# Kernel tuning notes

Measured on AMD Instinct MI355X. Metric: run time of the kernel, lower is better.

## Reference

```python
import jax, jax.numpy as jnp
import numpy as np
from jax import lax

CENTER_NUM = 2048


def setup_inputs() -> dict:
    key = jax.random.key(0)
    xyz = jax.random.normal(key, (32, 65536, 3), dtype=jnp.float32)
    return {"xyz": xyz}


def furthest_point_sample(xyz, m):
    """Iterative FPS. xyz: [B, N, 3] -> indices [B, m] (int32).

    Matches pointnet2_utils.furthest_point_sample: start at index 0,
    maintain running min squared distance to the selected set, pick argmax.
    """
    B, N, _ = xyz.shape
    init_idx = jnp.zeros((B,), dtype=jnp.int32)
    init_dists = jnp.full((B, N), 1e10, dtype=xyz.dtype)

    def step(carry, _):
        dists, last_idx = carry
        last = jnp.take_along_axis(xyz, last_idx[:, None, None], axis=1)  # [B,1,3]
        d = jnp.sum((xyz - last) ** 2, axis=-1)  # [B,N] squared dist to last center
        dists = jnp.minimum(dists, d)
        nxt = jnp.argmax(dists, axis=-1).astype(jnp.int32)  # [B]
        return (dists, nxt), nxt

    (_, _), rest = lax.scan(step, (init_dists, init_idx), None, length=m - 1)
    # rest: [m-1, B] -> prepend initial index, transpose to [B, m]
    idx = jnp.concatenate([init_idx[None, :], rest], axis=0).T
    return idx


def index_points(points, idx):
    """points: [B, N, C], idx: [B, m] -> [B, m, C]."""
    return jnp.take_along_axis(points, idx[..., None], axis=1)


def reference(xyz):
    fps_idx = furthest_point_sample(xyz, CENTER_NUM)  # [B, m]
    center_xyz = index_points(xyz, fps_idx)           # [B, m, 3]
    return center_xyz
```

## Files before the change

### kernel.cpp

```cpp
#include <hip/hip_runtime.h>
#include <stdint.h>

#define NBATCH 32
#define NPTS   65536
#define MCENT  2048
#define BPB    8
#define THREADS 1024
#define CHUNK  (NPTS / BPB)
#define WPT    (CHUNK / THREADS)
#define NWAVE  (THREADS / 64)
#define TMAX   64

typedef unsigned long long u64;
typedef uint32_t u32;

static __device__ __forceinline__ u32 fbits(float f) { union { float f; u32 u; } c; c.f = f; return c.u; }
static __device__ __forceinline__ float bitsf(u32 u) { union { u32 u; float f; } c; c.u = u; return c.f; }

static __device__ __forceinline__ u32 wave_max_u32(u32 v) {
#define STEP(CTRL) { const u32 o = (u32)__builtin_amdgcn_update_dpp(0, (int)v, CTRL, 0xF, 0xF, true); v = o > v ? o : v; }
    STEP(0x111)
    STEP(0x112)
    STEP(0x114)
    STEP(0x118)
    STEP(0x142)
    STEP(0x143)
#undef STEP
    return (u32)__builtin_amdgcn_readlane((int)v, 63);
}


template<int GPW>
__global__ __launch_bounds__(THREADS, 1) void fps_kernel(
    const float* __restrict__ xyz,
    float* __restrict__ out,
    u64* __restrict__ slots)
{
    constexpr int GROUPL = 64 / GPW;
    constexpr int POOLW  = BPB * NWAVE * GPW * 2;
    constexpr int WPL    = POOLW / 64;

    const int t = threadIdx.x;
    const int b = blockIdx.x >> 3;
    const int j = blockIdx.x & 7;
    const float* base = xyz + (size_t)b * NPTS * 3;
    const int p0 = j * CHUNK;
    const int wave = t >> 6;
    const int lane = t & 63;

    float px[WPT], py[WPT], pz[WPT], pd[WPT];
#pragma unroll
    for (int q = 0; q < WPT; ++q) {
        const int p = p0 + q * THREADS + t;
        px[q] = base[(size_t)p * 3 + 0];
        py[q] = base[(size_t)p * 3 + 1];
        pz[q] = base[(size_t)p * 3 + 2];
        pd[q] = 1e10f;
    }

    __shared__ float wcx[TMAX], wcy[TMAX], wcz[TMAX];
    __shared__ int   wcnt;

    if (t == 0) {
        const float cx = base[0], cy = base[1], cz = base[2];
        wcx[0] = cx; wcy[0] = cy; wcz[0] = cz; wcnt = 1;
        if (j == 0) {
            float* o = out + (size_t)b * MCENT * 3;
            o[0] = cx; o[1] = cy; o[2] = cz;
        }
    }

    int C = 0;
    for (int s = 1; ; ++s) {
        __syncthreads();
        const int tn = wcnt;
        C += tn;
        if (C >= MCENT) break;

        for (int tt = 0; tt < tn; ++tt) {
            const float cx = wcx[tt], cy = wcy[tt], cz = wcz[tt];
#pragma unroll
            for (int q = 0; q < WPT; ++q) {
                const float dx = __fsub_rn(px[q], cx);
                const float dy = __fsub_rn(py[q], cy);
                const float dz = __fsub_rn(pz[q], cz);
                const float s2 = __fmaf_rn(dz, dz,
                                 __fmaf_rn(dx, dx,
                                 __fmul_rn(dy, dy)));
                pd[q] = fminf(pd[q], s2);
            }
        }

        u64 k1 = 0, k2 = 0;
#pragma unroll
        for (int q = 0; q < WPT; ++q) {
            const u64 kk = ((u64)fbits(pd[q]) << 16)
                         | (u64)(0xFFFFu ^ (u32)(p0 + q * THREADS + t));
            if (kk > k1) { k2 = k1; k1 = kk; } else if (kk > k2) { k2 = kk; }
        }
#pragma unroll
        for (int m = 1; m <= GROUPL / 2; m <<= 1) {
            const u64 o1 = __shfl_xor(k1, m);
            const u64 o2 = __shfl_xor(k2, m);
            if (o1 > k1) { k2 = (k1 > o2) ? k1 : o2; k1 = o1; }
            else         { k2 = (k2 > o1) ? k2 : o1; }
        }

        u64* const bb = slots + ((size_t)(s & 1) * NBATCH + b) * POOLW;
        const u32 tag = (u32)s & 0xFFFFu;

        if ((lane & (GROUPL - 1)) == 0) {
            const int g = wave * GPW + lane / GROUPL;
            __hip_atomic_store(&bb[j * (NWAVE * GPW * 2) + g * 2 + 0],
                               (k1 << 16) | tag,
                               __ATOMIC_RELAXED, __HIP_MEMORY_SCOPE_AGENT);
            __hip_atomic_store(&bb[j * (NWAVE * GPW * 2) + g * 2 + 1],
                               (k2 << 16) | tag,
                               __ATOMIC_RELAXED, __HIP_MEMORY_SCOPE_AGENT);
        }

        if (wave == 0) {
            u64 w[WPL]; int ok;
            do {
#pragma unroll
                for (int r = 0; r < WPL; ++r)
                    w[r] = __hip_atomic_load(&bb[lane + 64 * r],
                                             __ATOMIC_RELAXED, __HIP_MEMORY_SCOPE_AGENT);
                ok = 1;
#pragma unroll
                for (int r = 0; r < WPL; ++r)
                    ok &= ((u32)(w[r] & 0xFFFFull) == tag);
            } while (!__all(ok));

            u32 pv[WPL], pi[WPL];
            float ex[WPL], ey[WPL], ez[WPL];
#pragma unroll
            for (int r = 0; r < WPL; ++r) {
                pv[r] = (u32)(w[r] >> 32);
                pi[r] = ((u32)w[r] >> 16) & 0xFFFFu;
                const int gi = (int)(0xFFFFu ^ pi[r]);
                ex[r] = base[(size_t)gi * 3 + 0];
                ey[r] = base[(size_t)gi * 3 + 1];
                ez[r] = base[(size_t)gi * 3 + 2];
            }

            u32 tl = 0;
#pragma unroll
            for (int r = 0; r < WPL; ++r) tl = pv[r] > tl ? pv[r] : tl;
            tl = (lane & 1) ? tl : 0u;
            const u32 tauv = wave_max_u32(tl);

            int tc = 0;
            while (1) {
                u32 lv = 0;
#pragma unroll
                for (int r = 0; r < WPL; ++r) lv = pv[r] > lv ? pv[r] : lv;
                const u32 vmax = wave_max_u32(lv);
                if (tc > 0 && vmax <= tauv) break;

                u32 ic = 0;
#pragma unroll
                for (int r = 0; r < WPL; ++r)
                    ic = (pv[r] == vmax && pi[r] + 1u > ic) ? pi[r] + 1u : ic;
                const u32 winv = wave_max_u32(ic) - 1u;

                float sx = 0.f, sy = 0.f, sz = 0.f; int mm = 0;
#pragma unroll
                for (int r = 0; r < WPL; ++r) {
                    const int m = (pv[r] == vmax) & (pi[r] == winv);
                    mm |= m;
                    sx = m ? ex[r] : sx;
                    sy = m ? ey[r] : sy;
                    sz = m ? ez[r] : sz;
                }
                const u64 bal = __ballot(mm);
                const int ol = (int)__ffsll((long long)bal) - 1;
                const float wx = __shfl(sx, ol);
                const float wy = __shfl(sy, ol);
                const float wz = __shfl(sz, ol);

                if (lane == 0) {
                    wcx[tc] = wx; wcy[tc] = wy; wcz[tc] = wz;
                    if (j == 0) {
                        float* o = out + ((size_t)b * MCENT + (C + tc)) * 3;
                        o[0] = wx; o[1] = wy; o[2] = wz;
                    }
                }
                ++tc;
                if (C + tc >= MCENT || tc >= TMAX) break;

#pragma unroll
                for (int r = 0; r < WPL; ++r) {
                    const float dx = __fsub_rn(ex[r], wx);
                    const float dy = __fsub_rn(ey[r], wy);
                    const float dz = __fsub_rn(ez[r], wz);
                    const float s2 = __fmaf_rn(dz, dz,
                                     __fmaf_rn(dx, dx,
                                     __fmul_rn(dy, dy)));
                    pv[r] = fbits(fminf(bitsf(pv[r]), s2));
                }
            }
            if (lane == 0) wcnt = tc;
        }
    }
}

extern "C" void kernel_launch(void* const* d_in, const int* in_sizes, int n_in,
                              void* d_out, int out_size, void* d_ws, size_t ws_size,
                              hipStream_t stream) {
    const float* xyz = (const float*)d_in[0];
    float* out = (float*)d_out;
    u64* slots = (u64*)d_ws;

    const size_t need_deep = 2ull * NBATCH * (BPB * NWAVE * 2 * 2) * sizeof(u64);
    if (ws_size >= need_deep) {
        fps_kernel<2><<<dim3(NBATCH * BPB), dim3(THREADS), 0, stream>>>(xyz, out, slots);
    } else {
        fps_kernel<1><<<dim3(NBATCH * BPB), dim3(THREADS), 0, stream>>>(xyz, out, slots);
    }
}
```

Before: 2.090 ms.

## Publish top-3 candidates per group to extract more centers per sync round

Each 32-lane group now keeps and merges a top-3 (instead of top-2) of its running-min distances and writes all three to the cross-block candidate pool. The pooled threshold is the max of the third-ranked entries, which should let more centers be selected per global synchronization round and so cut the number of inter-block barriers. It also adds a fast path for the winner lookup when only one lane holds the maximum, skipping a wave reduction. The cost is a heavier per-thread and per-shuffle merge, a larger pool for wave 0 to load and scan, and more stores per round.

```diff
diff --git a/kernel.cpp b/kernel.cpp
--- a/kernel.cpp
+++ b/kernel.cpp
@@ -9,6 +9,8 @@
 #define CHUNK  (NPTS / BPB)
 #define WPT    (CHUNK / THREADS)
 #define NWAVE  (THREADS / 64)
+#define GPW    2
+#define NGRP   (NWAVE * GPW)
 #define TMAX   64
 
 typedef unsigned long long u64;
@@ -30,15 +32,14 @@
 }
 
 
-template<int GPW>
+template<int TOPK>
 __global__ __launch_bounds__(THREADS, 1) void fps_kernel(
     const float* __restrict__ xyz,
     float* __restrict__ out,
     u64* __restrict__ slots)
 {
-    constexpr int GROUPL = 64 / GPW;
-    constexpr int POOLW  = BPB * NWAVE * GPW * 2;
-    constexpr int WPL    = POOLW / 64;
+    constexpr int POOLW = BPB * NGRP * TOPK;
+    constexpr int WPL   = POOLW / 64;
 
     const int t = threadIdx.x;
     const int b = blockIdx.x >> 3;
@@ -91,32 +92,51 @@
             }
         }
 
-        u64 k1 = 0, k2 = 0;
+        u64 k1 = 0, k2 = 0, k3 = 0;
 #pragma unroll
         for (int q = 0; q < WPT; ++q) {
             const u64 kk = ((u64)fbits(pd[q]) << 16)
                          | (u64)(0xFFFFu ^ (u32)(p0 + q * THREADS + t));
-            if (kk > k1) { k2 = k1; k1 = kk; } else if (kk > k2) { k2 = kk; }
-        }
-#pragma unroll
-        for (int m = 1; m <= GROUPL / 2; m <<= 1) {
+            if (kk > k1)      { k3 = k2; k2 = k1; k1 = kk; }
+            else if (kk > k2) { k3 = k2; k2 = kk; }
+            else if (kk > k3) { k3 = kk; }
+        }
+#pragma unroll
+        for (int m = 1; m <= 16; m <<= 1) {
             const u64 o1 = __shfl_xor(k1, m);
             const u64 o2 = __shfl_xor(k2, m);
-            if (o1 > k1) { k2 = (k1 > o2) ? k1 : o2; k1 = o1; }
-            else         { k2 = (k2 > o1) ? k2 : o1; }
+            if constexpr (TOPK == 2) {
+                if (o1 > k1) { k2 = (k1 > o2) ? k1 : o2; k1 = o1; }
+                else         { k2 = (k2 > o1) ? k2 : o1; }
+            } else {
+                const u64 o3 = __shfl_xor(k3, m);
+                u64 m1, m2, m3;
+                if (o1 > k1) {
+                    m1 = o1;
+                    if (o2 > k1) { m2 = o2; m3 = (o3 > k1) ? o3 : k1; }
+                    else         { m2 = k1; m3 = (o2 > k2) ? o2 : k2; }
+                } else {
+                    m1 = k1;
+                    if (o1 > k2) { m2 = o1; m3 = (o2 > k2) ? o2 : k2; }
+                    else         { m2 = k2; m3 = (o1 > k3) ? o1 : k3; }
+                }
+                k1 = m1; k2 = m2; k3 = m3;
+            }
         }
 
         u64* const bb = slots + ((size_t)(s & 1) * NBATCH + b) * POOLW;
         const u32 tag = (u32)s & 0xFFFFu;
 
-        if ((lane & (GROUPL - 1)) == 0) {
-            const int g = wave * GPW + lane / GROUPL;
-            __hip_atomic_store(&bb[j * (NWAVE * GPW * 2) + g * 2 + 0],
-                               (k1 << 16) | tag,
+        if ((lane & 31) == 0) {
+            const int g = wave * GPW + (lane >> 5);
+            u64* const gw = &bb[j * (NGRP * TOPK) + g * TOPK];
+            __hip_atomic_store(&gw[0], (k1 << 16) | tag,
                                __ATOMIC_RELAXED, __HIP_MEMORY_SCOPE_AGENT);
-            __hip_atomic_store(&bb[j * (NWAVE * GPW * 2) + g * 2 + 1],
-                               (k2 << 16) | tag,
+            __hip_atomic_store(&gw[1], (k2 << 16) | tag,
                                __ATOMIC_RELAXED, __HIP_MEMORY_SCOPE_AGENT);
+            if constexpr (TOPK == 3)
+                __hip_atomic_store(&gw[2], (k3 << 16) | tag,
+                                   __ATOMIC_RELAXED, __HIP_MEMORY_SCOPE_AGENT);
         }
 
         if (wave == 0) {
@@ -146,8 +166,10 @@
 
             u32 tl = 0;
 #pragma unroll
-            for (int r = 0; r < WPL; ++r) tl = pv[r] > tl ? pv[r] : tl;
-            tl = (lane & 1) ? tl : 0u;
+            for (int r = 0; r < WPL; ++r) {
+                const int rank = ((lane % TOPK) + (64 % TOPK) * r) % TOPK;
+                if (rank == TOPK - 1) tl = pv[r] > tl ? pv[r] : tl;
+            }
             const u32 tauv = wave_max_u32(tl);
 
             int tc = 0;
@@ -162,19 +184,28 @@
 #pragma unroll
                 for (int r = 0; r < WPL; ++r)
                     ic = (pv[r] == vmax && pi[r] + 1u > ic) ? pi[r] + 1u : ic;
-                const u32 winv = wave_max_u32(ic) - 1u;
-
-                float sx = 0.f, sy = 0.f, sz = 0.f; int mm = 0;
+                const u64 bal = __ballot(ic != 0);
+                u32 winv; int ol;
+                if (__popcll(bal) == 1) {
+                    ol = (int)__ffsll((long long)bal) - 1;
+                    winv = __shfl(ic, ol) - 1u;
+                } else {
+                    winv = wave_max_u32(ic) - 1u;
+                    int m = 0;
+#pragma unroll
+                    for (int r = 0; r < WPL; ++r)
+                        m |= (pv[r] == vmax) & (pi[r] == winv);
+                    ol = (int)__ffsll((long long)__ballot(m)) - 1;
+                }
+
+                float sx = 0.f, sy = 0.f, sz = 0.f;
 #pragma unroll
                 for (int r = 0; r < WPL; ++r) {
                     const int m = (pv[r] == vmax) & (pi[r] == winv);
-                    mm |= m;
                     sx = m ? ex[r] : sx;
                     sy = m ? ey[r] : sy;
                     sz = m ? ez[r] : sz;
                 }
-                const u64 bal = __ballot(mm);
-                const int ol = (int)__ffsll((long long)bal) - 1;
                 const float wx = __shfl(sx, ol);
                 const float wy = __shfl(sy, ol);
                 const float wz = __shfl(sz, ol);
@@ -212,10 +243,10 @@
     float* out = (float*)d_out;
     u64* slots = (u64*)d_ws;
 
-    const size_t need_deep = 2ull * NBATCH * (BPB * NWAVE * 2 * 2) * sizeof(u64);
-    if (ws_size >= need_deep) {
+    const size_t need3 = 2ull * NBATCH * (BPB * NGRP * 3) * sizeof(u64);
+    if (ws_size >= need3) {
+        fps_kernel<3><<<dim3(NBATCH * BPB), dim3(THREADS), 0, stream>>>(xyz, out, slots);
+    } else {
         fps_kernel<2><<<dim3(NBATCH * BPB), dim3(THREADS), 0, stream>>>(xyz, out, slots);
-    } else {
-        fps_kernel<1><<<dim3(NBATCH * BPB), dim3(THREADS), 0, stream>>>(xyz, out, slots);
     }
 }
```

After: 2.055 ms. About the same (-1.7%).
